# Performance work log

Hardware: AMD Instinct MI355X
Metric: run time of the kernel (lower is better)

The kernel has to match this reference:

```python
import jax, jax.numpy as jnp
import numpy as np

DEPTH, HEADS, DIM, DIM_HEAD, MLP = 2, 8, 512, 64, 2048
INNER = HEADS * DIM_HEAD  # == DIM here, but project_out is still True since dim_head != dim
NEG = -1e9


def _ln(t, g, b):
    mu = t.mean(-1, keepdims=True)
    var = ((t - mu) ** 2).mean(-1, keepdims=True)
    return (t - mu) / jnp.sqrt(var + 1e-5) * g + b


def _heads(t):
    b, n, hd = t.shape
    return t.reshape(b, n, HEADS, hd // HEADS).transpose(0, 2, 1, 3)  # b h n d


def _merge(t):
    b, h, n, d = t.shape
    return t.transpose(0, 2, 1, 3).reshape(b, n, h * d)


def kat_forward(x, kx, rd, clst, mask, kmask,
                ln1_g, ln1_b, Wqkv, Wout, bout, ln2_g, ln2_b, W1, b1, W2, b2):
    scale = DIM_HEAD ** -0.5
    # att_mask[b,1,n,m]: True where attention is disallowed (mask_i * kmask_j < 0.5)
    att_mask = (jnp.einsum('bid,bjd->bij', mask, kmask) < 0.5)[:, None]
    krd = rd[:, None]                      # [b,1,m,n]
    krdT = jnp.swapaxes(krd, -1, -2)       # [b,1,n,m]
    keep = (kmask >= 0.5)                  # kernel_mask fill-with-0 complement
    k_reps, atten = [], []
    for l in range(DEPTH):
        # pre-norm applied in-place before residual (as in the original)
        xn = _ln(x, ln1_g[l], ln1_b[l])
        kxn = _ln(kx, ln1_g[l], ln1_b[l])
        cn = _ln(clst, ln1_g[l], ln1_b[l])

        def qkv(t):
            q, k, v = jnp.split(t @ Wqkv[l], 3, axis=-1)
            return _heads(q), _heads(k), _heads(v)

        tq, tk, tv = qkv(xn)
        kq, kk, kv = qkv(kxn)
        cq, _, _ = qkv(cn)

        # patch -> kernel attention, krd-weighted dual softmax
        dots = jnp.einsum('bhid,bhjd->bhij', tq, kk) * scale      # [b,h,n,m]
        dots = jnp.where(att_mask, NEG, dots)
        attn_t = jax.nn.softmax(dots * 24, -1) * krdT             # temperature branch (attention map out)
        attn = jax.nn.softmax(dots, -1) * krdT
        x_ = _merge(jnp.einsum('bhij,bhjd->bhid', attn, kv)) @ Wout[l] + bout[l]

        # kernel -> patch attention
        kd = jnp.einsum('bhid,bhjd->bhij', kq, tk) * scale        # [b,h,m,n]
        kd = jnp.where(jnp.swapaxes(att_mask, -1, -2), NEG, kd)
        kattn = jax.nn.softmax(kd, -1) * krd
        kx_ = _merge(jnp.einsum('bhij,bhjd->bhid', kattn, tv)) @ Wout[l] + bout[l]

        # class token -> kernel attention
        cd = jnp.einsum('bhid,bhjd->bhij', cq, kk) * scale        # [b,h,1,m]
        cd = jnp.where(att_mask[:, :, :1], NEG, cd)
        c_ = _merge(jnp.einsum('bhij,bhjd->bhid', jax.nn.softmax(cd, -1), kv)) @ Wout[l] + bout[l]

        x, kx, clst = xn + x_, kxn + kx_, cn + c_

        def ff(t):
            tn = _ln(t, ln2_g[l], ln2_b[l])
            return jax.nn.gelu(tn @ W1[l] + b1[l], approximate=False) @ W2[l] + b2[l]

        x, kx, clst = ff(x) + x, ff(kx) + kx, ff(clst) + clst
        k_reps.append(kx * keep)
        atten.append(jnp.swapaxes(attn_t, -1, -2))  # [b,h,m,n]
    return jnp.stack(k_reps), clst, jnp.stack(atten)


def setup_inputs() -> dict:
    key = jax.random.key(0)
    ks = jax.random.split(key, 16)
    b, n, m = 4, 2048, 256
    s = 0.02
    L = DEPTH
    return {
        'x': jax.random.normal(ks[0], (b, n, DIM), jnp.float32),
        'kx': jax.random.normal(ks[1], (b, m, DIM), jnp.float32),
        'rd': jax.random.uniform(ks[2], (b, m, n), jnp.float32),
        'clst': jax.random.normal(ks[3], (b, 1, DIM), jnp.float32),
        'mask': jnp.ones((b, n, 1), jnp.float32),
        'kmask': jax.random.uniform(ks[4], (b, m, 1), jnp.float32),
        'ln1_g': jnp.ones((L, DIM), jnp.float32),
        'ln1_b': jnp.zeros((L, DIM), jnp.float32),
        'Wqkv': s * jax.random.normal(ks[5], (L, DIM, 3 * INNER), jnp.float32),
        'Wout': s * jax.random.normal(ks[6], (L, INNER, DIM), jnp.float32),
        'bout': jnp.zeros((L, DIM), jnp.float32),
        'ln2_g': jnp.ones((L, DIM), jnp.float32),
        'ln2_b': jnp.zeros((L, DIM), jnp.float32),
        'W1': s * jax.random.normal(ks[7], (L, DIM, MLP), jnp.float32),
        'b1': jnp.zeros((L, MLP), jnp.float32),
        'W2': s * jax.random.normal(ks[8], (L, MLP, DIM), jnp.float32),
        'b2': jnp.zeros((L, DIM), jnp.float32),
    }


def reference(x, kx, rd, clst, mask, kmask, ln1_g, ln1_b, Wqkv, Wout, bout,
              ln2_g, ln2_b, W1, b1, W2, b2):
    return kat_forward(x, kx, rd, clst, mask, kmask, ln1_g, ln1_b, Wqkv, Wout,
                       bout, ln2_g, ln2_b, W1, b1, W2, b2)
```

## Files before the change

kernel.cpp:

```cpp
#include <hip/hip_runtime.h>
#include <hip/hip_bf16.h>
#include <cstddef>

#define DEV __device__ __forceinline__

constexpr int Bb  = 4;
constexpr int Nn  = 2048;
constexpr int MK  = 256;
constexpr int Dd  = 512;
constexpr int Hh  = 8;
constexpr int DH  = 64;
constexpr int QLD = 1536;
constexpr int MLPD = 2048;
constexpr int NTOK = Bb * Nn + Bb * MK + Bb;
constexpr int KXOFF = Bb * Nn;
constexpr int CLOFF = Bb * Nn + Bb * MK;
constexpr float SCALE = 0.125f;
constexpr float NEGV  = -1e9f;

typedef __attribute__((ext_vector_type(8))) short short8;
typedef __attribute__((ext_vector_type(4))) float f32x4;

DEV float4 ldf4(const float* p) { return *reinterpret_cast<const float4*>(p); }

DEV void gload16(const short* g, short* l) {
  __builtin_amdgcn_global_load_lds(
      (const __attribute__((address_space(1))) void*)g,
      (__attribute__((address_space(3))) void*)l, 16, 0, 0);
}

DEV float waveMax(float v) {
#pragma unroll
  for (int o = 32; o; o >>= 1) v = fmaxf(v, __shfl_xor(v, o));
  return v;
}
DEV float waveSum(float v) {
#pragma unroll
  for (int o = 32; o; o >>= 1) v += __shfl_xor(v, o);
  return v;
}
DEV float blockMax256(float v, float* red) {
  v = waveMax(v);
  __syncthreads();
  if ((threadIdx.x & 63) == 0) red[threadIdx.x >> 6] = v;
  __syncthreads();
  return fmaxf(fmaxf(red[0], red[1]), fmaxf(red[2], red[3]));
}
DEV float blockSum256(float v, float* red) {
  v = waveSum(v);
  __syncthreads();
  if ((threadIdx.x & 63) == 0) red[threadIdx.x >> 6] = v;
  __syncthreads();
  return red[0] + red[1] + red[2] + red[3];
}
DEV float gelu_f(float x) { return 0.5f * x * (1.f + erff(x * 0.70710678118654752f)); }
DEV float pow24(float e1) {
  float e2 = e1 * e1, e4 = e2 * e2, e8 = e4 * e4, e16 = e8 * e8;
  return e16 * e8;
}
DEV short bf16bits(float v) {
  __hip_bfloat16 h = __float2bfloat16(v);
  return *reinterpret_cast<short*>(&h);
}

__global__ __launch_bounds__(256)
void copy3_kernel(const float* __restrict__ x, const float* __restrict__ kx,
                  const float* __restrict__ c, float* __restrict__ dst) {
  const int idx = blockIdx.x * 256 + threadIdx.x;
  const int row = idx >> 7;
  float4 v;
  if (row < KXOFF) v = ldf4(x + (size_t)idx * 4);
  else if (row < CLOFF) v = ldf4(kx + (size_t)idx * 4 - (size_t)KXOFF * Dd);
  else v = ldf4(c + (size_t)idx * 4 - (size_t)CLOFF * Dd);
  *reinterpret_cast<float4*>(dst + (size_t)idx * 4) = v;
}

__global__ __launch_bounds__(64)
void ln_kernel(const float* __restrict__ in, const float* __restrict__ gw,
               const float* __restrict__ bw, __hip_bfloat16* __restrict__ outb) {
  const int row = blockIdx.x;
  const int t = threadIdx.x;
  const float* p = in + (size_t)row * Dd + t * 8;
  float4 v0 = ldf4(p), v1 = ldf4(p + 4);
  float s = v0.x + v0.y + v0.z + v0.w + v1.x + v1.y + v1.z + v1.w;
  float q = v0.x*v0.x + v0.y*v0.y + v0.z*v0.z + v0.w*v0.w
          + v1.x*v1.x + v1.y*v1.y + v1.z*v1.z + v1.w*v1.w;
  s = waveSum(s); q = waveSum(q);
  const float mu = s * (1.f / Dd);
  const float rstd = rsqrtf(fmaxf(q * (1.f / Dd) - mu * mu, 0.f) + 1e-5f);
  float4 g0 = ldf4(gw + t * 8), g1 = ldf4(gw + t * 8 + 4);
  float4 b0 = ldf4(bw + t * 8), b1 = ldf4(bw + t * 8 + 4);
  float o[8];
  o[0] = (v0.x - mu) * rstd * g0.x + b0.x;
  o[1] = (v0.y - mu) * rstd * g0.y + b0.y;
  o[2] = (v0.z - mu) * rstd * g0.z + b0.z;
  o[3] = (v0.w - mu) * rstd * g0.w + b0.w;
  o[4] = (v1.x - mu) * rstd * g1.x + b1.x;
  o[5] = (v1.y - mu) * rstd * g1.y + b1.y;
  o[6] = (v1.z - mu) * rstd * g1.z + b1.z;
  o[7] = (v1.w - mu) * rstd * g1.w + b1.w;
  __hip_bfloat16* ob = outb + (size_t)row * Dd + t * 8;
#pragma unroll
  for (int e = 0; e < 8; ++e) ob[e] = __float2bfloat16(o[e]);
}

struct GArgs {
  const short* A;  long asb; int lda;
  const short* Bt; long bsb; int ldb;
  float* C; __hip_bfloat16* Cb;
  long czo, czi; int ldc;
  const float* bias;
  const float* res; const __hip_bfloat16* resb; int ldr;
  float* out2; const float* km2;
  int M, N, K;
};

template<int BM, int BN, int EPI>
__global__ __launch_bounds__(256)
void mgemm(GArgs g) {
  constexpr int WMW = (BN >= 128) ? 2 : 4;
  constexpr int WNW = 4 / WMW;
  constexpr int WM = BM / WMW, WN = BN / WNW;
  constexpr int FM = WM / 16, FN = WN / 16;
  __shared__ __align__(16) short As[BM * 64];
  __shared__ __align__(16) short Bs[BN * 64];
  const int tid = threadIdx.x, l = tid & 63, w = tid >> 6;
  const int wm = (WNW == 2) ? (w >> 1) : w;
  const int wn = (WNW == 2) ? (w & 1) : 0;
  int bx = blockIdx.x, by = blockIdx.y;
  {
    const int gx = gridDim.x, nwg = gx * gridDim.y;
    const int orig = by * gx + bx;
    const int xcd = orig & 7, pos = orig >> 3;
    const int q = nwg >> 3, rmd = nwg & 7;
    const int s = (xcd < rmd ? xcd * (q + 1) : rmd * (q + 1) + (xcd - rmd) * q) + pos;
    bx = s % gx; by = s / gx;
  }
  const int z = blockIdx.z;
  const short* Ab = g.A + (size_t)z * g.asb;
  const short* Bb_ = g.Bt + (size_t)z * g.bsb;
  f32x4 acc[FM][FN] = {};
  const int lr = l & 15, lg = l >> 4;

  for (int k0 = 0; k0 < g.K; k0 += 64) {
    __syncthreads();
#pragma unroll
    for (int it = 0; it < BM / 32; ++it) {
      int idx = tid + it * 256, r = idx >> 3, c = idx & 7;
      int gm = by * BM + r;
      if (gm >= g.M) gm = g.M - 1;
      gload16(Ab + (size_t)gm * g.lda + k0 + ((c ^ (r & 7)) * 8), As + idx * 8);
    }
#pragma unroll
    for (int it = 0; it < BN / 32; ++it) {
      int idx = tid + it * 256, r = idx >> 3, c = idx & 7;
      int gn = bx * BN + r;
      gload16(Bb_ + (size_t)gn * g.ldb + k0 + ((c ^ (r & 7)) * 8), Bs + idx * 8);
    }
    __syncthreads();
#pragma unroll
    for (int ks = 0; ks < 2; ++ks) {
      short8 a[FM], b[FN];
#pragma unroll
      for (int fm = 0; fm < FM; ++fm) {
        int rr = wm * WM + fm * 16 + lr;
        int ch = (ks * 4 + lg) ^ (rr & 7);
        a[fm] = *reinterpret_cast<const short8*>(As + rr * 64 + ch * 8);
      }
#pragma unroll
      for (int fn = 0; fn < FN; ++fn) {
        int rn = wn * WN + fn * 16 + lr;
        int ch = (ks * 4 + lg) ^ (rn & 7);
        b[fn] = *reinterpret_cast<const short8*>(Bs + rn * 64 + ch * 8);
      }
#pragma unroll
      for (int fm = 0; fm < FM; ++fm)
#pragma unroll
        for (int fn = 0; fn < FN; ++fn)
          acc[fm][fn] = __builtin_amdgcn_mfma_f32_16x16x32_bf16(a[fm], b[fn], acc[fm][fn], 0, 0, 0);
    }
  }

  const size_t zoff = (size_t)(z >> 3) * g.czo + (size_t)(z & 7) * g.czi;
#pragma unroll
  for (int fm = 0; fm < FM; ++fm) {
#pragma unroll
    for (int fn = 0; fn < FN; ++fn) {
#pragma unroll
      for (int r = 0; r < 4; ++r) {
        int m = by * BM + wm * WM + fm * 16 + lg * 4 + r;
        int n = bx * BN + wn * WN + fn * 16 + lr;
        if (m >= g.M) continue;
        float v = acc[fm][fn][r];
        size_t coff = zoff + (size_t)m * g.ldc + n;
        if (EPI == 0) {
          g.C[coff] = v;
        } else if (EPI == 2) {
          v += g.bias[n] + g.res[(size_t)m * g.ldr + n];
          g.C[coff] = v;
        } else if (EPI == 5) {
          v += g.bias[n] + __bfloat162float(g.resb[(size_t)m * g.ldr + n]);
          g.C[coff] = v;
        } else if (EPI == 6) {
          v += g.bias[n] + g.res[(size_t)m * g.ldr + n];
          g.C[coff] = v;
          if (m >= KXOFF && m < CLOFF) {
            int t = m - KXOFF;
            float keep = (g.km2[t] >= 0.5f) ? 1.f : 0.f;
            g.out2[(size_t)t * Dd + n] = v * keep;
          }
        } else if (EPI == 3) {
          v = gelu_f(v + g.bias[n]);
          g.Cb[coff] = __float2bfloat16(v);
        } else {
          g.Cb[coff] = __float2bfloat16(v);
        }
      }
    }
  }
}

template<int BM, int BN, int EPI>
static void launch_mgemm(const GArgs& g, int zdim, hipStream_t s) {
  dim3 grid((g.N + BN - 1) / BN, (g.M + BM - 1) / BM, zdim);
  mgemm<BM, BN, EPI><<<grid, 256, 0, s>>>(g);
}

struct QArgs {
  const short* A; int lda;
  const short* Bt; int ldb;
  __hip_bfloat16 *tq, *tk, *kq, *kk, *tvT, *kvT;
  float* cq;
  int M, K;
};

__global__ __launch_bounds__(256)
void qkv_gemm(QArgs g) {
  __shared__ __align__(16) char smem[34816];
  short* As = (short*)smem;
  short* Bs = (short*)(smem + 16384);
  short* tb = (short*)smem;
  const int tid = threadIdx.x, l = tid & 63, w = tid >> 6;
  const int wm = w >> 1, wn = w & 1;
  int bx = blockIdx.x, by = blockIdx.y;
  {
    const int gx = gridDim.x, nwg = gx * gridDim.y;
    const int orig = by * gx + bx;
    const int xcd = orig & 7, pos = orig >> 3;
    const int q = nwg >> 3, rmd = nwg & 7;
    const int s = (xcd < rmd ? xcd * (q + 1) : rmd * (q + 1) + (xcd - rmd) * q) + pos;
    bx = s % gx; by = s / gx;
  }
  f32x4 acc[4][4] = {};
  const int lr = l & 15, lg = l >> 4;

  for (int k0 = 0; k0 < g.K; k0 += 64) {
    __syncthreads();
#pragma unroll
    for (int it = 0; it < 4; ++it) {
      int idx = tid + it * 256, r = idx >> 3, c = idx & 7;
      int gm = by * 128 + r;
      if (gm >= g.M) gm = g.M - 1;
      gload16(g.A + (size_t)gm * g.lda + k0 + ((c ^ (r & 7)) * 8), As + idx * 8);
    }
#pragma unroll
    for (int it = 0; it < 4; ++it) {
      int idx = tid + it * 256, r = idx >> 3, c = idx & 7;
      int gn = bx * 128 + r;
      gload16(g.Bt + (size_t)gn * g.ldb + k0 + ((c ^ (r & 7)) * 8), Bs + idx * 8);
    }
    __syncthreads();
#pragma unroll
    for (int ks = 0; ks < 2; ++ks) {
      short8 a[4], b[4];
#pragma unroll
      for (int fm = 0; fm < 4; ++fm) {
        int rr = wm * 64 + fm * 16 + lr;
        int ch = (ks * 4 + lg) ^ (rr & 7);
        a[fm] = *reinterpret_cast<const short8*>(As + rr * 64 + ch * 8);
      }
#pragma unroll
      for (int fn = 0; fn < 4; ++fn) {
        int rn = wn * 64 + fn * 16 + lr;
        int ch = (ks * 4 + lg) ^ (rn & 7);
        b[fn] = *reinterpret_cast<const short8*>(Bs + rn * 64 + ch * 8);
      }
#pragma unroll
      for (int fm = 0; fm < 4; ++fm)
#pragma unroll
        for (int fn = 0; fn < 4; ++fn)
          acc[fm][fn] = __builtin_amdgcn_mfma_f32_16x16x32_bf16(a[fm], b[fn], acc[fm][fn], 0, 0, 0);
    }
  }

  const int sec = bx >> 2;
  const int region = (by < 64) ? 0 : (by < 72 ? 1 : 2);

  if (sec == 2) {
    if (region == 2) return;
    __syncthreads();
#pragma unroll
    for (int fm = 0; fm < 4; ++fm)
#pragma unroll
      for (int fn = 0; fn < 4; ++fn)
#pragma unroll
        for (int r = 0; r < 4; ++r) {
          int mloc = wm * 64 + fm * 16 + lg * 4 + r;
          int nloc = wn * 64 + fn * 16 + lr;
          tb[nloc * 136 + mloc] = bf16bits(acc[fm][fn][r]);
        }
    __syncthreads();
    const int nloc = tid >> 1, mh = (tid & 1) * 64;
    const int nv = (bx - 8) * 128 + nloc;
    const int h = nv >> 6, d = nv & 63;
    int T, b, ibase;
    __hip_bfloat16* vT;
    if (region == 0) {
      T = Nn; b = by >> 4; ibase = (by & 15) * 128 + mh; vT = g.tvT;
    } else {
      T = MK; int t0 = (by - 64) * 128 + mh; b = t0 >> 8; ibase = t0 & 255; vT = g.kvT;
    }
    short* dst = (short*)vT + ((size_t)(b * 8 + h) * 64 + d) * T + ibase;
    const short* src = tb + nloc * 136 + mh;
#pragma unroll
    for (int e = 0; e < 8; ++e)
      *reinterpret_cast<short8*>(dst + e * 8) = *reinterpret_cast<const short8*>(src + e * 8);
    return;
  }

  if (region == 2) {
    if (sec == 0) {
#pragma unroll
      for (int fm = 0; fm < 4; ++fm)
#pragma unroll
        for (int fn = 0; fn < 4; ++fn)
#pragma unroll
          for (int r = 0; r < 4; ++r) {
            int m = by * 128 + wm * 64 + fm * 16 + lg * 4 + r;
            if (m >= g.M) continue;
            int n = bx * 128 + wn * 64 + fn * 16 + lr;
            g.cq[(size_t)(m - CLOFF) * Dd + n] = acc[fm][fn][r];
          }
    }
    return;
  }

  const int T = region ? MK : Nn;
#pragma unroll
  for (int fm = 0; fm < 4; ++fm) {
#pragma unroll
    for (int fn = 0; fn < 4; ++fn) {
#pragma unroll
      for (int r = 0; r < 4; ++r) {
        int m = by * 128 + wm * 64 + fm * 16 + lg * 4 + r;
        int n = bx * 128 + wn * 64 + fn * 16 + lr;
        float v = acc[fm][fn][r];
        int t = region ? m - KXOFF : m;
        int b = region ? (t >> 8) : (t >> 11);
        int i = region ? (t & 255) : (t & 2047);
        int h = (n >> 6) & 7, d = n & 63;
        size_t tok = (size_t)(b * 8 + h) * T + i;
        if (sec == 0) {
          if (region == 0) {
            __hip_bfloat16 hi = __float2bfloat16(v);
            g.tq[tok * 128 + d] = hi;
            g.tq[tok * 128 + 64 + d] = __float2bfloat16(v - __bfloat162float(hi));
          } else {
            g.kq[tok * 64 + d] = __float2bfloat16(v);
          }
        } else {
          if (region == 0) {
            g.tk[tok * 64 + d] = __float2bfloat16(v);
          } else {
            __hip_bfloat16 hi = __float2bfloat16(v);
            g.kk[tok * 128 + d] = hi;
            g.kk[tok * 128 + 64 + d] = __float2bfloat16(v - __bfloat162float(hi));
          }
        }
      }
    }
  }
}

__global__ __launch_bounds__(512)
void score_sx_kernel(const short* __restrict__ Q, const short* __restrict__ Km,
                     const float* __restrict__ mask, const float* __restrict__ kmask,
                     const float* __restrict__ rdT,
                     __hip_bfloat16* __restrict__ P1, float* __restrict__ atten) {
  __shared__ __align__(16) char smem[49152];
  short* As = (short*)smem;
  short* Bs = (short*)(smem + 16384);
  float* tb = (float*)smem;
  __shared__ float red[128 * 2];
  __shared__ float red2[128 * 4];
  const int tid = threadIdx.x, l = tid & 63, w = tid >> 6;
  const int wm = w >> 1, wn = w & 1;
  const int by = blockIdx.x, bh = blockIdx.y;
  const int b = bh >> 3;
  const short* Ab = Q + (size_t)bh * Nn * 128;
  const short* Bb = Km + (size_t)bh * MK * 128;
  const int lr = l & 15, lg = l >> 4;
  f32x4 acc[2][8] = {};

  for (int k0 = 0; k0 < 128; k0 += 64) {
    __syncthreads();
#pragma unroll
    for (int it = 0; it < 2; ++it) {
      int idx = tid + it * 512, r = idx >> 3, c = idx & 7;
      gload16(Ab + (size_t)(by * 128 + r) * 128 + k0 + ((c ^ (r & 7)) * 8), As + idx * 8);
    }
#pragma unroll
    for (int it = 0; it < 4; ++it) {
      int idx = tid + it * 512, r = idx >> 3, c = idx & 7;
      gload16(Bb + (size_t)r * 128 + k0 + ((c ^ (r & 7)) * 8), Bs + idx * 8);
    }
    __syncthreads();
#pragma unroll
    for (int ks = 0; ks < 2; ++ks) {
      short8 a[2], bv[8];
#pragma unroll
      for (int fm = 0; fm < 2; ++fm) {
        int rr = wm * 32 + fm * 16 + lr;
        int ch = (ks * 4 + lg) ^ (rr & 7);
        a[fm] = *reinterpret_cast<const short8*>(As + rr * 64 + ch * 8);
      }
#pragma unroll
      for (int fn = 0; fn < 8; ++fn) {
        int rn = wn * 128 + fn * 16 + lr;
        int ch = (ks * 4 + lg) ^ (rn & 7);
        bv[fn] = *reinterpret_cast<const short8*>(Bs + rn * 64 + ch * 8);
      }
#pragma unroll
      for (int fm = 0; fm < 2; ++fm)
#pragma unroll
        for (int fn = 0; fn < 8; ++fn)
          acc[fm][fn] = __builtin_amdgcn_mfma_f32_16x16x32_bf16(a[fm], bv[fn], acc[fm][fn], 0, 0, 0);
    }
  }
  {
    float colm[8];
#pragma unroll
    for (int fn = 0; fn < 8; ++fn)
      colm[fn] = kmask[b * MK + wn * 128 + fn * 16 + lr];
#pragma unroll
    for (int fm = 0; fm < 2; ++fm)
#pragma unroll
      for (int r = 0; r < 4; ++r) {
        float rm = mask[(size_t)b * Nn + by * 128 + wm * 32 + fm * 16 + lg * 4 + r];
#pragma unroll
        for (int fn = 0; fn < 8; ++fn)
          acc[fm][fn][r] = (rm * colm[fn] < 0.5f) ? NEGV : acc[fm][fn][r] * SCALE;
      }
  }
  float mx[2][4];
#pragma unroll
  for (int fm = 0; fm < 2; ++fm)
#pragma unroll
    for (int r = 0; r < 4; ++r) {
      float m = -3.4e38f;
#pragma unroll
      for (int fn = 0; fn < 8; ++fn) m = fmaxf(m, acc[fm][fn][r]);
#pragma unroll
      for (int o = 8; o; o >>= 1) m = fmaxf(m, __shfl_xor(m, o));
      mx[fm][r] = m;
    }
  __syncthreads();
  if (lr == 0) {
#pragma unroll
    for (int fm = 0; fm < 2; ++fm)
#pragma unroll
      for (int r = 0; r < 4; ++r)
        red[(wm * 32 + fm * 16 + lg * 4 + r) * 2 + wn] = mx[fm][r];
  }
  __syncthreads();
#pragma unroll
  for (int fm = 0; fm < 2; ++fm)
#pragma unroll
    for (int r = 0; r < 4; ++r) {
      int row = wm * 32 + fm * 16 + lg * 4 + r;
      mx[fm][r] = fmaxf(red[row * 2], red[row * 2 + 1]);
    }
  float s1[2][4], s24[2][4];
#pragma unroll
  for (int fm = 0; fm < 2; ++fm)
#pragma unroll
    for (int r = 0; r < 4; ++r) {
      float a1 = 0.f, a24 = 0.f;
#pragma unroll
      for (int fn = 0; fn < 8; ++fn) {
        float e1 = __expf(acc[fm][fn][r] - mx[fm][r]);
        acc[fm][fn][r] = e1;
        a1 += e1;
        a24 += pow24(e1);
      }
#pragma unroll
      for (int o = 8; o; o >>= 1) { a1 += __shfl_xor(a1, o); a24 += __shfl_xor(a24, o); }
      s1[fm][r] = a1; s24[fm][r] = a24;
    }
  __syncthreads();
  if (lr == 0) {
#pragma unroll
    for (int fm = 0; fm < 2; ++fm)
#pragma unroll
      for (int r = 0; r < 4; ++r) {
        int row = wm * 32 + fm * 16 + lg * 4 + r;
        red2[row * 4 + wn * 2]     = s1[fm][r];
        red2[row * 4 + wn * 2 + 1] = s24[fm][r];
      }
  }
  __syncthreads();
#pragma unroll
  for (int fm = 0; fm < 2; ++fm)
#pragma unroll
    for (int r = 0; r < 4; ++r) {
      int row = wm * 32 + fm * 16 + lg * 4 + r;
      s1[fm][r]  = 1.f / (red2[row * 4] + red2[row * 4 + 2]);
      s24[fm][r] = 1.f / (red2[row * 4 + 1] + red2[row * 4 + 3]);
    }
#pragma unroll
  for (int fm = 0; fm < 2; ++fm) {
#pragma unroll
    for (int r = 0; r < 4; ++r) {
      int m = by * 128 + wm * 32 + fm * 16 + lg * 4 + r;
      const float* rp = rdT + ((size_t)b * Nn + m) * MK;
      size_t obase = ((size_t)bh * Nn + m) * MK;
#pragma unroll
      for (int fn = 0; fn < 8; ++fn) {
        int n = wn * 128 + fn * 16 + lr;
        float e1 = acc[fm][fn][r];
        float rv = rp[n];
        P1[obase + n] = __float2bfloat16(e1 * s1[fm][r] * rv);
        acc[fm][fn][r] = pow24(e1) * s24[fm][r] * rv;
      }
    }
  }
  const int jw = tid >> 1, ipw = (tid & 1) * 16;
#pragma unroll
  for (int c = 0; c < 4; ++c) {
    __syncthreads();
    if (wm == c) {
#pragma unroll
      for (int fm = 0; fm < 2; ++fm)
#pragma unroll
        for (int r = 0; r < 4; ++r) {
          int mloc = fm * 16 + lg * 4 + r;
#pragma unroll
          for (int fn = 0; fn < 8; ++fn) {
            int n = wn * 128 + fn * 16 + lr;
            tb[n * 33 + mloc] = acc[fm][fn][r];
          }
        }
    }
    __syncthreads();
    float* op = atten + ((size_t)bh * MK + jw) * Nn + by * 128 + c * 32 + ipw;
    const float* tp = tb + jw * 33 + ipw;
#pragma unroll
    for (int e = 0; e < 4; ++e)
      *reinterpret_cast<float4*>(op + e * 4) =
          make_float4(tp[e * 4], tp[e * 4 + 1], tp[e * 4 + 2], tp[e * 4 + 3]);
  }
}

__global__ __launch_bounds__(256)
void score_sk_kernel(const short* __restrict__ Qk, const short* __restrict__ Kt,
                     const float* __restrict__ mask, const float* __restrict__ kmask,
                     const float* __restrict__ rd, __hip_bfloat16* __restrict__ P2) {
  __shared__ __align__(16) short As[16 * 64];
  __shared__ __align__(16) short Bs[256 * 64];
  __shared__ float redm[16 * 4];
  __shared__ float reds[16 * 4];
  const int tid = threadIdx.x, l = tid & 63, w = tid >> 6;
  const int lr = l & 15, lg = l >> 4;
  const int bh = blockIdx.x, j0 = blockIdx.y * 16, b = bh >> 3;
  const short* Ab = Qk + ((size_t)bh * MK + j0) * 64;
  const short* Bb = Kt + (size_t)bh * Nn * 64;
  f32x4 acc[32];
#pragma unroll
  for (int q = 0; q < 32; ++q) acc[q] = f32x4{0.f, 0.f, 0.f, 0.f};
  if (tid < 128) {
    int r = tid >> 3, c = tid & 7;
    gload16(Ab + (size_t)r * 64 + ((c ^ (r & 7)) * 8), As + tid * 8);
  }
#pragma unroll
  for (int nc = 0; nc < 8; ++nc) {
    __syncthreads();
#pragma unroll
    for (int it = 0; it < 8; ++it) {
      int idx = tid + it * 256, r = idx >> 3, c = idx & 7;
      gload16(Bb + (size_t)(nc * 256 + r) * 64 + ((c ^ (r & 7)) * 8), Bs + idx * 8);
    }
    __syncthreads();
#pragma unroll
    for (int ks = 0; ks < 2; ++ks) {
      short8 a;
      {
        int ch = (ks * 4 + lg) ^ (lr & 7);
        a = *reinterpret_cast<const short8*>(As + lr * 64 + ch * 8);
      }
#pragma unroll
      for (int fn = 0; fn < 4; ++fn) {
        int rn = w * 64 + fn * 16 + lr;
        int ch = (ks * 4 + lg) ^ (rn & 7);
        short8 bv = *reinterpret_cast<const short8*>(Bs + rn * 64 + ch * 8);
        acc[nc * 4 + fn] =
            __builtin_amdgcn_mfma_f32_16x16x32_bf16(a, bv, acc[nc * 4 + fn], 0, 0, 0);
      }
    }
  }
  float rm[4];
#pragma unroll
  for (int rr = 0; rr < 4; ++rr) rm[rr] = kmask[b * MK + j0 + lg * 4 + rr];
  float mx[4] = {-3.4e38f, -3.4e38f, -3.4e38f, -3.4e38f};
#pragma unroll
  for (int q = 0; q < 32; ++q) {
    int n = (q >> 2) * 256 + w * 64 + (q & 3) * 16 + lr;
    float cm = mask[(size_t)b * Nn + n];
#pragma unroll
    for (int rr = 0; rr < 4; ++rr) {
      float v = (rm[rr] * cm < 0.5f) ? NEGV : acc[q][rr] * SCALE;
      acc[q][rr] = v;
      mx[rr] = fmaxf(mx[rr], v);
    }
  }
#pragma unroll
  for (int o = 8; o; o >>= 1)
#pragma unroll
    for (int rr = 0; rr < 4; ++rr) mx[rr] = fmaxf(mx[rr], __shfl_xor(mx[rr], o));
  __syncthreads();
  if (lr == 0) {
#pragma unroll
    for (int rr = 0; rr < 4; ++rr) redm[(lg * 4 + rr) * 4 + w] = mx[rr];
  }
  __syncthreads();
#pragma unroll
  for (int rr = 0; rr < 4; ++rr) {
    int row = lg * 4 + rr;
    mx[rr] = fmaxf(fmaxf(redm[row * 4], redm[row * 4 + 1]),
                   fmaxf(redm[row * 4 + 2], redm[row * 4 + 3]));
  }
  float sm[4] = {0.f, 0.f, 0.f, 0.f};
#pragma unroll
  for (int q = 0; q < 32; ++q)
#pragma unroll
    for (int rr = 0; rr < 4; ++rr) {
      float e = __expf(acc[q][rr] - mx[rr]);
      acc[q][rr] = e;
      sm[rr] += e;
    }
#pragma unroll
  for (int o = 8; o; o >>= 1)
#pragma unroll
    for (int rr = 0; rr < 4; ++rr) sm[rr] += __shfl_xor(sm[rr], o);
  __syncthreads();
  if (lr == 0) {
#pragma unroll
    for (int rr = 0; rr < 4; ++rr) reds[(lg * 4 + rr) * 4 + w] = sm[rr];
  }
  __syncthreads();
  float inv[4];
#pragma unroll
  for (int rr = 0; rr < 4; ++rr) {
    int row = lg * 4 + rr;
    inv[rr] = 1.f / (reds[row * 4] + reds[row * 4 + 1] + reds[row * 4 + 2] + reds[row * 4 + 3]);
  }
#pragma unroll
  for (int rr = 0; rr < 4; ++rr) {
    int j = j0 + lg * 4 + rr;
    const float* rp = rd + (size_t)(b * MK + j) * Nn;
    __hip_bfloat16* pp = P2 + ((size_t)bh * MK + j) * Nn;
#pragma unroll
    for (int q = 0; q < 32; ++q) {
      int n = (q >> 2) * 256 + w * 64 + (q & 3) * 16 + lr;
      pp[n] = __float2bfloat16(acc[q][rr] * inv[rr] * rp[n]);
    }
  }
}

__global__ __launch_bounds__(256)
void rd_tr_kernel(const float* __restrict__ rd, float* __restrict__ rdT) {
  __shared__ float tb[64][65];
  const int b = blockIdx.x;
  const int i0 = blockIdx.y * 64, j0 = blockIdx.z * 64;
  const int tid = threadIdx.x;
#pragma unroll
  for (int it = 0; it < 4; ++it) {
    int idx = tid + it * 256, r = idx >> 4, c4 = (idx & 15) * 4;
    float4 v = ldf4(rd + ((size_t)(b * MK + j0 + r)) * Nn + i0 + c4);
    tb[r][c4 + 0] = v.x; tb[r][c4 + 1] = v.y; tb[r][c4 + 2] = v.z; tb[r][c4 + 3] = v.w;
  }
  __syncthreads();
#pragma unroll
  for (int it = 0; it < 4; ++it) {
    int idx = tid + it * 256, r = idx >> 4, c4 = (idx & 15) * 4;
    float4 o = make_float4(tb[c4 + 0][r], tb[c4 + 1][r], tb[c4 + 2][r], tb[c4 + 3][r]);
    *reinterpret_cast<float4*>(rdT + ((size_t)(b * Nn + i0 + r)) * MK + j0 + c4) = o;
  }
}

struct WtArgs {
  const float* W[8];
  __hip_bfloat16* T[8];
  int K[8], N[8];
};
__global__ __launch_bounds__(256)
void wtrans_all_kernel(WtArgs a) {
  __shared__ float t[64][65];
  const int e = blockIdx.z;
  const int K = a.K[e], N = a.N[e];
  const int n0 = blockIdx.x * 64, k0 = blockIdx.y * 64;
  if (n0 >= N || k0 >= K) return;
  const float* W = a.W[e];
  __hip_bfloat16* WT = a.T[e];
  const int tid = threadIdx.x;
#pragma unroll
  for (int it = 0; it < 4; ++it) {
    int idx = tid + it * 256, r = idx >> 4, f = idx & 15;
    float4 v = ldf4(W + (size_t)(k0 + r) * N + n0 + f * 4);
    t[r][f * 4 + 0] = v.x; t[r][f * 4 + 1] = v.y;
    t[r][f * 4 + 2] = v.z; t[r][f * 4 + 3] = v.w;
  }
  __syncthreads();
#pragma unroll
  for (int it = 0; it < 4; ++it) {
    int idx = tid + it * 256, r = idx >> 4, c4 = (idx & 15) * 4;
    __hip_bfloat16* op = WT + (size_t)(n0 + r) * K + k0 + c4;
#pragma unroll
    for (int e2 = 0; e2 < 4; ++e2) op[e2] = __float2bfloat16(t[c4 + e2][r]);
  }
}

__global__ __launch_bounds__(256)
void attn_c_kernel(const float* __restrict__ cq, const __hip_bfloat16* __restrict__ kk,
                   const __hip_bfloat16* __restrict__ kvT,
                   const float* __restrict__ mask, const float* __restrict__ kmask,
                   __hip_bfloat16* __restrict__ c_pre) {
  __shared__ __align__(16) float kv_s[MK][DH];
  __shared__ __align__(16) float q_s[DH];
  __shared__ float pbuf[MK];
  __shared__ float red8[8];
  __shared__ float redpv[4][DH];
  const int tid = threadIdx.x;
  const int bh = blockIdx.x, b = bh >> 3, h = bh & 7;
#pragma unroll
  for (int d = 0; d < DH; ++d)
    kv_s[tid][d] = __bfloat162float(kvT[((size_t)(b * 8 + h) * 64 + d) * MK + tid]);
  if (tid < DH) q_s[tid] = cq[(size_t)b * Dd + h * DH + tid];
  __syncthreads();
  const __hip_bfloat16* kp = kk + ((size_t)((b * 8 + h) * MK + tid)) * 128;
  float dot = 0.f;
#pragma unroll
  for (int d = 0; d < DH; ++d) {
    float kd = __bfloat162float(kp[d]) + __bfloat162float(kp[64 + d]);
    dot = fmaf(q_s[d], kd, dot);
  }
  const float dm = (mask[(size_t)b * Nn] * kmask[b * MK + tid] < 0.5f) ? NEGV : dot * SCALE;
  const float mx = blockMax256(dm, red8);
  const float e = __expf(dm - mx);
  const float s = blockSum256(e, red8);
  pbuf[tid] = e / s;
  __syncthreads();
  const int d = tid & 63, g = tid >> 6;
  float acc = 0.f;
#pragma unroll 8
  for (int jj = 0; jj < 64; ++jj)
    acc = fmaf(pbuf[g * 64 + jj], kv_s[g * 64 + jj][d], acc);
  redpv[g][d] = acc;
  __syncthreads();
  if (tid < DH)
    c_pre[(size_t)b * Dd + h * DH + tid] = __float2bfloat16(
        redpv[0][tid] + redpv[1][tid] + redpv[2][tid] + redpv[3][tid]);
}

__global__ void cout_kernel(const float* __restrict__ c_s, float* __restrict__ o) {
  const int idx = blockIdx.x * 256 + threadIdx.x;
  o[idx] = c_s[idx];
}

static GArgs ga_base() { GArgs g = {}; return g; }

extern "C" void kernel_launch(void* const* d_in, const int* in_sizes, int n_in,
                              void* d_out, int out_size, void* d_ws, size_t ws_size,
                              hipStream_t stream) {
  (void)in_sizes; (void)n_in; (void)out_size; (void)ws_size;
  const float* x_in  = (const float*)d_in[0];
  const float* kx_in = (const float*)d_in[1];
  const float* rd    = (const float*)d_in[2];
  const float* c_in  = (const float*)d_in[3];
  const float* mask  = (const float*)d_in[4];
  const float* kmask = (const float*)d_in[5];
  const float* ln1g  = (const float*)d_in[6];
  const float* ln1b  = (const float*)d_in[7];
  const float* Wqkv  = (const float*)d_in[8];
  const float* Woutw = (const float*)d_in[9];
  const float* boutw = (const float*)d_in[10];
  const float* ln2g  = (const float*)d_in[11];
  const float* ln2b  = (const float*)d_in[12];
  const float* W1    = (const float*)d_in[13];
  const float* b1    = (const float*)d_in[14];
  const float* W2    = (const float*)d_in[15];
  const float* b2    = (const float*)d_in[16];
  float* out = (float*)d_out;

  float* ws = (float*)d_ws;
  size_t off = 0;
  auto alloc = [&](size_t n) { float* p = ws + off; off += (n + 15) & ~(size_t)15; return p; };
  float* xcat_s    = alloc((size_t)NTOK * Dd);
  float* xcat_nb_f = alloc((size_t)NTOK * Dd / 2);
  float* pre_cat_f = alloc((size_t)NTOK * Dd / 2);
  float* hid_f     = alloc((size_t)NTOK * MLPD / 2);
  float* cq        = alloc((size_t)Bb * Dd);
  float* P1_f      = alloc((size_t)32 * Nn * MK / 2);
  float* P2_f      = alloc((size_t)32 * MK * Nn / 2);
  float* tq_s_f    = alloc((size_t)32 * Nn * 128 / 2);
  float* kk_s_f    = alloc((size_t)32 * MK * 128 / 2);
  float* tk_hi_f   = alloc((size_t)32 * Nn * 64 / 2);
  float* kq_hi_f   = alloc((size_t)32 * MK * 64 / 2);
  float* tvT_f     = alloc((size_t)32 * 64 * Nn / 2);
  float* kvT_f     = alloc((size_t)32 * 64 * MK / 2);
  float* rdT       = alloc((size_t)Bb * Nn * MK);
  float* WqkvT_f   = alloc((size_t)2 * QLD * Dd / 2);
  float* WoutT_f   = alloc((size_t)2 * Dd * Dd / 2);
  float* W1T_f     = alloc((size_t)2 * MLPD * Dd / 2);
  float* W2T_f     = alloc((size_t)2 * Dd * MLPD / 2);

  __hip_bfloat16* xcat_nb = (__hip_bfloat16*)xcat_nb_f;
  __hip_bfloat16* pre_cat = (__hip_bfloat16*)pre_cat_f;
  __hip_bfloat16* hid     = (__hip_bfloat16*)hid_f;
  __hip_bfloat16* P1b     = (__hip_bfloat16*)P1_f;
  __hip_bfloat16* P2b     = (__hip_bfloat16*)P2_f;
  __hip_bfloat16* tq_s    = (__hip_bfloat16*)tq_s_f;
  __hip_bfloat16* kk_s    = (__hip_bfloat16*)kk_s_f;
  __hip_bfloat16* tk_hi   = (__hip_bfloat16*)tk_hi_f;
  __hip_bfloat16* kq_hi   = (__hip_bfloat16*)kq_hi_f;
  __hip_bfloat16* tvT     = (__hip_bfloat16*)tvT_f;
  __hip_bfloat16* kvT     = (__hip_bfloat16*)kvT_f;
  __hip_bfloat16* WqkvT   = (__hip_bfloat16*)WqkvT_f;
  __hip_bfloat16* WoutT   = (__hip_bfloat16*)WoutT_f;
  __hip_bfloat16* W1T     = (__hip_bfloat16*)W1T_f;
  __hip_bfloat16* W2T     = (__hip_bfloat16*)W2T_f;

  const size_t CL_OFF = (size_t)2 * Bb * MK * Dd;
  const size_t AT_OFF = CL_OFF + (size_t)Bb * Dd;

  copy3_kernel<<<(NTOK * 128) / 256, 256, 0, stream>>>(x_in, kx_in, c_in, xcat_s);
  rd_tr_kernel<<<dim3(Bb, Nn / 64, MK / 64), 256, 0, stream>>>(rd, rdT);
  {
    WtArgs a;
    for (int l = 0; l < 2; ++l) {
      a.W[l * 4 + 0] = Wqkv + (size_t)l * Dd * QLD;  a.T[l * 4 + 0] = WqkvT + (size_t)l * QLD * Dd;
      a.K[l * 4 + 0] = Dd;   a.N[l * 4 + 0] = QLD;
      a.W[l * 4 + 1] = Woutw + (size_t)l * Dd * Dd;  a.T[l * 4 + 1] = WoutT + (size_t)l * Dd * Dd;
      a.K[l * 4 + 1] = Dd;   a.N[l * 4 + 1] = Dd;
      a.W[l * 4 + 2] = W1 + (size_t)l * Dd * MLPD;   a.T[l * 4 + 2] = W1T + (size_t)l * MLPD * Dd;
      a.K[l * 4 + 2] = Dd;   a.N[l * 4 + 2] = MLPD;
      a.W[l * 4 + 3] = W2 + (size_t)l * MLPD * Dd;   a.T[l * 4 + 3] = W2T + (size_t)l * Dd * MLPD;
      a.K[l * 4 + 3] = MLPD; a.N[l * 4 + 3] = Dd;
    }
    wtrans_all_kernel<<<dim3(32, 32, 8), 256, 0, stream>>>(a);
  }

  for (int l = 0; l < 2; ++l) {
    const float* bo  = boutw + (size_t)l * Dd;
    const float* b1l = b1 + (size_t)l * MLPD;
    const float* b2l = b2 + (size_t)l * Dd;
    __hip_bfloat16* WqkvTl = WqkvT + (size_t)l * QLD * Dd;
    __hip_bfloat16* WoutTl = WoutT + (size_t)l * Dd * Dd;
    __hip_bfloat16* W1Tl   = W1T + (size_t)l * MLPD * Dd;
    __hip_bfloat16* W2Tl   = W2T + (size_t)l * Dd * MLPD;

    ln_kernel<<<NTOK, 64, 0, stream>>>(xcat_s, ln1g + l * Dd, ln1b + l * Dd, xcat_nb);

    {
      QArgs q = {};
      q.A = (const short*)xcat_nb; q.lda = Dd;
      q.Bt = (const short*)WqkvTl; q.ldb = Dd;
      q.tq = tq_s; q.tk = tk_hi; q.kq = kq_hi; q.kk = kk_s;
      q.tvT = tvT; q.kvT = kvT; q.cq = cq;
      q.M = NTOK; q.K = Dd;
      qkv_gemm<<<dim3(QLD / 128, (NTOK + 127) / 128, 1), 256, 0, stream>>>(q);
    }

    attn_c_kernel<<<Bb * Hh, 256, 0, stream>>>(cq, kk_s, kvT, mask, kmask,
                                               pre_cat + (size_t)CLOFF * Dd);

    score_sx_kernel<<<dim3(Nn / 128, 32), 512, 0, stream>>>(
        (const short*)tq_s, (const short*)kk_s, mask, kmask, rdT, P1b,
        out + AT_OFF + (size_t)l * 32 * MK * Nn);
    {
      GArgs g = ga_base();
      g.A = (const short*)P1b; g.asb = (long)Nn * MK; g.lda = MK;
      g.Bt = (const short*)kvT; g.bsb = (long)64 * MK; g.ldb = MK;
      g.Cb = pre_cat; g.czo = (long)Nn * Dd; g.czi = 64; g.ldc = Dd;
      g.M = Nn; g.N = 64; g.K = MK;
      launch_mgemm<128, 64, 4>(g, 32, stream);
    }
    score_sk_kernel<<<dim3(32, MK / 16), 256, 0, stream>>>(
        (const short*)kq_hi, (const short*)tk_hi, mask, kmask, rd, P2b);
    {
      GArgs g = ga_base();
      g.A = (const short*)P2b; g.asb = (long)MK * Nn; g.lda = Nn;
      g.Bt = (const short*)tvT; g.bsb = (long)64 * Nn; g.ldb = Nn;
      g.Cb = pre_cat + (size_t)KXOFF * Dd; g.czo = (long)MK * Dd; g.czi = 64; g.ldc = Dd;
      g.M = MK; g.N = 64; g.K = Nn;
      launch_mgemm<64, 64, 4>(g, 32, stream);
    }

    {
      GArgs g = ga_base();
      g.A = (const short*)pre_cat; g.lda = Dd;
      g.Bt = (const short*)WoutTl; g.ldb = Dd;
      g.C = xcat_s; g.ldc = Dd; g.bias = bo; g.resb = xcat_nb; g.ldr = Dd;
      g.M = NTOK; g.N = Dd; g.K = Dd;
      launch_mgemm<128, 64, 5>(g, 1, stream);
    }

    ln_kernel<<<NTOK, 64, 0, stream>>>(xcat_s, ln2g + l * Dd, ln2b + l * Dd, xcat_nb);
    {
      GArgs g = ga_base();
      g.A = (const short*)xcat_nb; g.lda = Dd;
      g.Bt = (const short*)W1Tl; g.ldb = Dd;
      g.Cb = hid; g.ldc = MLPD; g.bias = b1l;
      g.M = NTOK; g.N = MLPD; g.K = Dd;
      launch_mgemm<128, 128, 3>(g, 1, stream);
      GArgs h = ga_base();
      h.A = (const short*)hid; h.lda = MLPD;
      h.Bt = (const short*)W2Tl; h.ldb = MLPD;
      h.C = xcat_s; h.ldc = Dd; h.bias = b2l; h.res = xcat_s; h.ldr = Dd;
      h.out2 = out + (size_t)l * Bb * MK * Dd; h.km2 = kmask;
      h.M = NTOK; h.N = Dd; h.K = MLPD;
      launch_mgemm<128, 64, 6>(h, 1, stream);
    }
  }
  cout_kernel<<<(Bb * Dd) / 256, 256, 0, stream>>>(xcat_s + (size_t)CLOFF * Dd, out + CL_OFF);
}
```

Before: 653.2 us.

## Triple-buffer GEMM LDS tiles with async prefetch two stages ahead

Rewrites the shared bf16 MFMA GEMM main loop to use three LDS buffers. Global-to-LDS loads are issued two K-tiles ahead and gated with explicit vmcnt waits and raw s_barrier instead of a load-then-sync loop. The goal is to hide global memory latency behind MFMA work. LDS use triples, which can lower occupancy, so the W1 GEMM tile is also shrunk from 128x128 to 128x64.

```diff
diff --git a/kernel.cpp b/kernel.cpp
--- a/kernel.cpp
+++ b/kernel.cpp
@@ -27,6 +27,11 @@
   __builtin_amdgcn_global_load_lds(
       (const __attribute__((address_space(1))) void*)g,
       (__attribute__((address_space(3))) void*)l, 16, 0, 0);
+}
+DEV void sbar() { __builtin_amdgcn_s_barrier(); }
+DEV void schedbar() { __builtin_amdgcn_sched_barrier(0); }
+constexpr int wc_imm(int vm) {
+  return (vm & 15) | (((vm >> 4) & 3) << 14) | (7 << 4) | (15 << 8);
 }
 
 DEV float waveMax(float v) {
@@ -122,8 +127,9 @@
   constexpr int WNW = 4 / WMW;
   constexpr int WM = BM / WMW, WN = BN / WNW;
   constexpr int FM = WM / 16, FN = WN / 16;
-  __shared__ __align__(16) short As[BM * 64];
-  __shared__ __align__(16) short Bs[BN * 64];
+  constexpr int LA = BM / 32, LB = BN / 32, LT = LA + LB;
+  __shared__ __align__(16) short As[3][BM * 64];
+  __shared__ __align__(16) short Bs[3][BN * 64];
   const int tid = threadIdx.x, l = tid & 63, w = tid >> 6;
   const int wm = (WNW == 2) ? (w >> 1) : w;
   const int wn = (WNW == 2) ? (w & 1) : 0;
@@ -142,22 +148,36 @@
   f32x4 acc[FM][FN] = {};
   const int lr = l & 15, lg = l >> 4;
 
-  for (int k0 = 0; k0 < g.K; k0 += 64) {
-    __syncthreads();
-#pragma unroll
-    for (int it = 0; it < BM / 32; ++it) {
+  auto stage = [&](int t) {
+    const int buf = t % 3;
+    const int k0 = t << 6;
+#pragma unroll
+    for (int it = 0; it < LA; ++it) {
       int idx = tid + it * 256, r = idx >> 3, c = idx & 7;
       int gm = by * BM + r;
       if (gm >= g.M) gm = g.M - 1;
-      gload16(Ab + (size_t)gm * g.lda + k0 + ((c ^ (r & 7)) * 8), As + idx * 8);
-    }
-#pragma unroll
-    for (int it = 0; it < BN / 32; ++it) {
+      gload16(Ab + (size_t)gm * g.lda + k0 + ((c ^ (r & 7)) * 8), &As[buf][idx * 8]);
+    }
+#pragma unroll
+    for (int it = 0; it < LB; ++it) {
       int idx = tid + it * 256, r = idx >> 3, c = idx & 7;
       int gn = bx * BN + r;
-      gload16(Bb_ + (size_t)gn * g.ldb + k0 + ((c ^ (r & 7)) * 8), Bs + idx * 8);
-    }
-    __syncthreads();
+      gload16(Bb_ + (size_t)gn * g.ldb + k0 + ((c ^ (r & 7)) * 8), &Bs[buf][idx * 8]);
+    }
+  };
+
+  const int NT = g.K >> 6;
+  stage(0);
+  if (NT > 1) stage(1);
+  for (int t = 0; t < NT; ++t) {
+    if (t + 2 < NT) stage(t + 2);
+    schedbar();
+    if (t + 2 < NT)      __builtin_amdgcn_s_waitcnt(wc_imm(2 * LT));
+    else if (t + 1 < NT) __builtin_amdgcn_s_waitcnt(wc_imm(LT));
+    else                 __builtin_amdgcn_s_waitcnt(wc_imm(0));
+    sbar();
+    schedbar();
+    const int cur = t % 3;
 #pragma unroll
     for (int ks = 0; ks < 2; ++ks) {
       short8 a[FM], b[FN];
@@ -165,13 +185,13 @@
       for (int fm = 0; fm < FM; ++fm) {
         int rr = wm * WM + fm * 16 + lr;
         int ch = (ks * 4 + lg) ^ (rr & 7);
-        a[fm] = *reinterpret_cast<const short8*>(As + rr * 64 + ch * 8);
+        a[fm] = *reinterpret_cast<const short8*>(&As[cur][rr * 64 + ch * 8]);
       }
 #pragma unroll
       for (int fn = 0; fn < FN; ++fn) {
         int rn = wn * WN + fn * 16 + lr;
         int ch = (ks * 4 + lg) ^ (rn & 7);
-        b[fn] = *reinterpret_cast<const short8*>(Bs + rn * 64 + ch * 8);
+        b[fn] = *reinterpret_cast<const short8*>(&Bs[cur][rn * 64 + ch * 8]);
       }
 #pragma unroll
       for (int fm = 0; fm < FM; ++fm)
@@ -179,6 +199,9 @@
         for (int fn = 0; fn < FN; ++fn)
           acc[fm][fn] = __builtin_amdgcn_mfma_f32_16x16x32_bf16(a[fm], b[fn], acc[fm][fn], 0, 0, 0);
     }
+    schedbar();
+    sbar();
+    schedbar();
   }
 
   const size_t zoff = (size_t)(z >> 3) * g.czo + (size_t)(z & 7) * g.czi;
@@ -921,7 +944,7 @@
       g.Bt = (const short*)W1Tl; g.ldb = Dd;
       g.Cb = hid; g.ldc = MLPD; g.bias = b1l;
       g.M = NTOK; g.N = MLPD; g.K = Dd;
-      launch_mgemm<128, 128, 3>(g, 1, stream);
+      launch_mgemm<128, 64, 3>(g, 1, stream);
       GArgs h = ga_base();
       h.A = (const short*)hid; h.lda = MLPD;
       h.Bt = (const short*)W2Tl; h.ldb = MLPD;
```

Result: slower. 730.5 us (+11.8%).
